# Optimization experiments

Measured on AMD Instinct MI355X. Metric: run time of the kernel, lower is better.

The kernel has to match this reference:

```python
import jax, jax.numpy as jnp
import numpy as np

TEMPERATURE = 0.5
NEG_FILL = -9000000000000000.0


def setup_inputs() -> dict:
    key = jax.random.key(0)
    k1, k2 = jax.random.split(key)
    z1 = jax.random.normal(k1, (4096, 256), dtype=jnp.float32)
    z2 = jax.random.normal(k2, (4096, 256), dtype=jnp.float32)
    return {"z1": z1, "z2": z2}


def reference(z1, z2):
    N = z1.shape[0]
    z = jnp.concatenate([z1, z2], axis=0)  # [2N, d]
    # cosine similarity: normalize once (eps matches torch's 1e-8) then GEMM
    norm = jnp.maximum(jnp.linalg.norm(z, axis=-1, keepdims=True), 1e-8)
    zn = z / norm
    sim = (zn @ zn.T) / TEMPERATURE  # [2N, 2N]
    # mask out self-similarity on the diagonal
    diag = jnp.eye(2 * N, dtype=bool)
    sim = jnp.where(diag, NEG_FILL, sim)
    labels = jnp.concatenate([jnp.arange(N) + N, jnp.arange(N)])  # positive pairs
    logp = jax.nn.log_softmax(sim, axis=-1)
    loss = -jnp.mean(jnp.take_along_axis(logp, labels[:, None], axis=1))
    return loss
```

## Files before the change

kernel.cpp:

```cpp
#include <hip/hip_runtime.h>
#include <hip/hip_bf16.h>


#define TWO_N 8192
#define NPAIR 4096
#define DDIM  256
#define NT    64
#define NBLK  (NT * (NT + 1) / 2)
#define INV_T 2.0f

typedef __attribute__((ext_vector_type(8))) short bf16x8;
typedef __attribute__((ext_vector_type(4))) float f32x4;

typedef __attribute__((address_space(1))) void gvoid_t;
typedef __attribute__((address_space(3))) void lvoid_t;

__device__ __forceinline__ void gload_lds16(const void* g, void* l) {
    __builtin_amdgcn_global_load_lds((gvoid_t*)g, (lvoid_t*)l, 16, 0, 0);
}

__global__ void k_normalize(const float* __restrict__ z1,
                            const float* __restrict__ z2,
                            __hip_bfloat16* __restrict__ zn,
                            float* __restrict__ e_diag,
                            float* __restrict__ pos,
                            float* __restrict__ row_sumexp,
                            float* __restrict__ out) {
    if (threadIdx.x < 8) row_sumexp[blockIdx.x * 8 + threadIdx.x] = 0.0f;
    if (blockIdx.x == 0 && threadIdx.x == 0) out[0] = 0.0f;

    const int w    = threadIdx.x >> 6;
    const int lane = threadIdx.x & 63;
    const int i    = blockIdx.x * 4 + w;

    float4 a = ((const float4*)(z1 + (size_t)i * DDIM))[lane];
    float4 b = ((const float4*)(z2 + (size_t)i * DDIM))[lane];

    float s1 = a.x * a.x + a.y * a.y + a.z * a.z + a.w * a.w;
    float s2 = b.x * b.x + b.y * b.y + b.z * b.z + b.w * b.w;
    float dd = a.x * b.x + a.y * b.y + a.z * b.z + a.w * b.w;
#pragma unroll
    for (int m = 1; m < 64; m <<= 1) {
        s1 += __shfl_xor(s1, m, 64);
        s2 += __shfl_xor(s2, m, 64);
        dd += __shfl_xor(dd, m, 64);
    }

    float inv1 = 1.0f / fmaxf(sqrtf(s1), 1e-8f);
    float inv2 = 1.0f / fmaxf(sqrtf(s2), 1e-8f);

    __hip_bfloat16 q1[4], q2[4];
    q1[0] = __float2bfloat16(a.x * inv1); q1[1] = __float2bfloat16(a.y * inv1);
    q1[2] = __float2bfloat16(a.z * inv1); q1[3] = __float2bfloat16(a.w * inv1);
    q2[0] = __float2bfloat16(b.x * inv2); q2[1] = __float2bfloat16(b.y * inv2);
    q2[2] = __float2bfloat16(b.z * inv2); q2[3] = __float2bfloat16(b.w * inv2);

    float qs1 = 0.0f, qs2 = 0.0f;
#pragma unroll
    for (int j = 0; j < 4; ++j) {
        float f1 = __bfloat162float(q1[j]);
        float f2 = __bfloat162float(q2[j]);
        qs1 += f1 * f1;
        qs2 += f2 * f2;
    }
#pragma unroll
    for (int m = 1; m < 64; m <<= 1) {
        qs1 += __shfl_xor(qs1, m, 64);
        qs2 += __shfl_xor(qs2, m, 64);
    }

    *reinterpret_cast<uint2*>(zn + (size_t)i * DDIM + lane * 4) =
        *reinterpret_cast<uint2*>(q1);
    *reinterpret_cast<uint2*>(zn + (size_t)(i + NPAIR) * DDIM + lane * 4) =
        *reinterpret_cast<uint2*>(q2);

    if (lane == 0) {
        e_diag[i]         = __expf(qs1 * INV_T);
        e_diag[i + NPAIR] = __expf(qs2 * INV_T);
        pos[i]            = dd * inv1 * inv2 * INV_T;
    }
}

__global__ __launch_bounds__(256, 2)
void k_gemm_sumexp(const __hip_bfloat16* __restrict__ zn,
                   float* __restrict__ row_sumexp) {
    __shared__ __align__(128) __hip_bfloat16 Asmem[128 * DDIM];

    const int tid  = threadIdx.x;
    const int lane = tid & 63;
    const int w    = tid >> 6;
    const int wr   = w >> 1;
    const int wc   = w & 1;
    const int lr   = lane & 15;
    const int quad = lane >> 4;

    int b = (blockIdx.x & 7) * (NBLK / 8) + (blockIdx.x >> 3);

    int rt = (int)(64.5f - sqrtf(64.5f * 64.5f - 2.0f * (float)b));
    if (rt < 0) rt = 0;
    if (rt > NT - 1) rt = NT - 1;
    while (rt > 0 && NT * rt - (rt * (rt - 1)) / 2 > b) --rt;
    while (NT * (rt + 1) - ((rt + 1) * rt) / 2 <= b) ++rt;
    const int ct   = rt + (b - (NT * rt - (rt * (rt - 1)) / 2));
    const bool diag = (rt == ct);

    const int row_base = rt * 128;
    const int col_base = ct * 128;

    const __hip_bfloat16* gB[4];
#pragma unroll
    for (int ni = 0; ni < 4; ++ni)
        gB[ni] = zn + (size_t)(col_base + wc * 64 + ni * 16 + lr) * DDIM + quad * 8;

    bf16x8 Bfr[8][4];
#pragma unroll
    for (int ks = 0; ks < 8; ++ks)
#pragma unroll
        for (int ni = 0; ni < 4; ++ni)
            Bfr[ks][ni] = *(const bf16x8*)(gB[ni] + ks * 32);

    {
        const int ck = (tid & 24) | ((tid & 7) ^ (tid >> 5));
        const char* gA = (const char*)(zn + (size_t)row_base * DDIM)
                       + (tid >> 5) * (DDIM * 2) + ck * 16;
        char* lA = (char*)Asmem + tid * 16;
#pragma unroll
        for (int j = 0; j < 16; ++j)
            gload_lds16(gA + (size_t)j * 8 * (DDIM * 2), lA + j * 4096);
    }
    __syncthreads();

    int pa[4];
#pragma unroll
    for (int mi = 0; mi < 4; ++mi)
        pa[mi] = (wr * 64 + mi * 16 + lr) * (DDIM * 2) + ((quad ^ (lr & 7)) << 4);

    f32x4 acc[4][4];
#pragma unroll
    for (int mi = 0; mi < 4; ++mi)
#pragma unroll
        for (int ni = 0; ni < 4; ++ni) acc[mi][ni] = (f32x4){0.f, 0.f, 0.f, 0.f};

    bf16x8 afc[4];
#pragma unroll
    for (int mi = 0; mi < 4; ++mi)
        afc[mi] = *(const bf16x8*)((const char*)Asmem + pa[mi]);

#pragma unroll
    for (int kstep = 0; kstep < 8; ++kstep) {
        bf16x8 afn[4];
        if (kstep < 7) {
            const int kn   = kstep + 1;
            const int koff = ((kn >> 1) << 7);
            const int kx   = ((kn & 1) << 6);
#pragma unroll
            for (int mi = 0; mi < 4; ++mi)
                afn[mi] = *(const bf16x8*)((const char*)Asmem + ((pa[mi] ^ kx) + koff));
        }
#pragma unroll
        for (int mi = 0; mi < 4; ++mi)
#pragma unroll
            for (int ni = 0; ni < 4; ++ni)
                acc[mi][ni] = __builtin_amdgcn_mfma_f32_16x16x32_bf16(
                    afc[mi], Bfr[kstep][ni], acc[mi][ni], 0, 0, 0);
        if (kstep < 7) {
#pragma unroll
            for (int mi = 0; mi < 4; ++mi) afc[mi] = afn[mi];
        }
    }

    float rs[4][4];
    float cs[4];
#pragma unroll
    for (int mi = 0; mi < 4; ++mi)
#pragma unroll
        for (int r = 0; r < 4; ++r) rs[mi][r] = 0.0f;
#pragma unroll
    for (int ni = 0; ni < 4; ++ni) cs[ni] = 0.0f;

#pragma unroll
    for (int mi = 0; mi < 4; ++mi)
#pragma unroll
        for (int ni = 0; ni < 4; ++ni)
#pragma unroll
            for (int r = 0; r < 4; ++r) {
                float e = __expf(acc[mi][ni][r] * INV_T);
                rs[mi][r] += e;
                cs[ni] += e;
            }

#pragma unroll
    for (int mi = 0; mi < 4; ++mi) {
#pragma unroll
        for (int r = 0; r < 4; ++r) {
            float v = rs[mi][r];
            v += __shfl_xor(v, 1, 64);
            v += __shfl_xor(v, 2, 64);
            v += __shfl_xor(v, 4, 64);
            v += __shfl_xor(v, 8, 64);
            if (lr == 0) {
                int row = row_base + wr * 64 + mi * 16 + quad * 4 + r;
                atomicAdd(&row_sumexp[row], v);
            }
        }
    }

    if (!diag) {
#pragma unroll
        for (int ni = 0; ni < 4; ++ni) {
            float v = cs[ni];
            v += __shfl_xor(v, 16, 64);
            v += __shfl_xor(v, 32, 64);
            if (quad == 0) {
                int col = col_base + wc * 64 + ni * 16 + lr;
                atomicAdd(&row_sumexp[col], v);
            }
        }
    }
}

__global__ void k_final(const float* __restrict__ row_sumexp,
                        const float* __restrict__ e_diag,
                        const float* __restrict__ pos,
                        float* __restrict__ out) {
    const int i    = blockIdx.x * 256 + threadIdx.x;
    const int w    = threadIdx.x >> 6;
    const int lane = threadIdx.x & 63;

    float t = logf(row_sumexp[i] - e_diag[i])
            + logf(row_sumexp[i + NPAIR] - e_diag[i + NPAIR])
            - 2.0f * pos[i];
#pragma unroll
    for (int m = 1; m < 64; m <<= 1) t += __shfl_xor(t, m, 64);

    __shared__ float ps[4];
    if (lane == 0) ps[w] = t;
    __syncthreads();
    if (threadIdx.x == 0) {
        float s = (ps[0] + ps[1] + ps[2] + ps[3]) * (1.0f / (float)TWO_N);
        atomicAdd(out, s);
    }
}

extern "C" void kernel_launch(void* const* d_in, const int* in_sizes, int n_in,
                              void* d_out, int out_size, void* d_ws, size_t ws_size,
                              hipStream_t stream) {
    const float* z1 = (const float*)d_in[0];
    const float* z2 = (const float*)d_in[1];
    float* out = (float*)d_out;

    char* ws = (char*)d_ws;
    __hip_bfloat16* zn  = (__hip_bfloat16*)ws;
    float* row_sumexp   = (float*)(ws + (size_t)TWO_N * DDIM * 2);
    float* e_diag       = row_sumexp + TWO_N;
    float* pos          = e_diag + TWO_N;

    k_normalize<<<NPAIR / 4, 256, 0, stream>>>(z1, z2, zn, e_diag, pos,
                                               row_sumexp, out);
    k_gemm_sumexp<<<NBLK, 256, 0, stream>>>(zn, row_sumexp);
    k_final<<<NPAIR / 256, 256, 0, stream>>>(row_sumexp, e_diag, pos, out);
}
```

Before: 126.0 us.

## Make GEMM-sumexp kernel persistent with A-tile reuse and overlapped epilogue

Replaces one-block-per-tile launch with a fixed grid of 256 persistent 512-thread blocks, each walking a contiguous range of upper-triangular tiles. The A row tile is restaged into LDS only when the row index changes, so consecutive tiles in the same row reuse it. The previous tile's exp/atomic epilogue runs while the next tile's B fragments load through inline asm global loads with manual waitcnt. This aims to cut launch and tail overhead and redundant A loads, at the cost of hand-tuned waitcnt assumptions and possible load imbalance across blocks.

```diff
diff --git a/kernel.cpp b/kernel.cpp
--- a/kernel.cpp
+++ b/kernel.cpp
@@ -8,6 +8,7 @@
 #define NT    64
 #define NBLK  (NT * (NT + 1) / 2)
 #define INV_T 2.0f
+#define GEMM_GRID 256
 
 typedef __attribute__((ext_vector_type(8))) short bf16x8;
 typedef __attribute__((ext_vector_type(4))) float f32x4;
@@ -81,7 +82,7 @@
     }
 }
 
-__global__ __launch_bounds__(256, 2)
+__global__ __launch_bounds__(512, 2)
 void k_gemm_sumexp(const __hip_bfloat16* __restrict__ zn,
                    float* __restrict__ row_sumexp) {
     __shared__ __align__(128) __hip_bfloat16 Asmem[128 * DDIM];
@@ -89,134 +90,155 @@
     const int tid  = threadIdx.x;
     const int lane = tid & 63;
     const int w    = tid >> 6;
-    const int wr   = w >> 1;
-    const int wc   = w & 1;
+    const int wr   = w >> 2;
+    const int wc   = w & 3;
     const int lr   = lane & 15;
     const int quad = lane >> 4;
 
-    int b = (blockIdx.x & 7) * (NBLK / 8) + (blockIdx.x >> 3);
-
+    const int t0 = (blockIdx.x * NBLK) >> 8;
+    const int t1 = ((blockIdx.x + 1) * NBLK) >> 8;
+
+    int b = t0;
     int rt = (int)(64.5f - sqrtf(64.5f * 64.5f - 2.0f * (float)b));
     if (rt < 0) rt = 0;
     if (rt > NT - 1) rt = NT - 1;
     while (rt > 0 && NT * rt - (rt * (rt - 1)) / 2 > b) --rt;
     while (NT * (rt + 1) - ((rt + 1) * rt) / 2 <= b) ++rt;
-    const int ct   = rt + (b - (NT * rt - (rt * (rt - 1)) / 2));
-    const bool diag = (rt == ct);
-
-    const int row_base = rt * 128;
-    const int col_base = ct * 128;
-
-    const __hip_bfloat16* gB[4];
-#pragma unroll
-    for (int ni = 0; ni < 4; ++ni)
-        gB[ni] = zn + (size_t)(col_base + wc * 64 + ni * 16 + lr) * DDIM + quad * 8;
-
-    bf16x8 Bfr[8][4];
-#pragma unroll
-    for (int ks = 0; ks < 8; ++ks)
-#pragma unroll
-        for (int ni = 0; ni < 4; ++ni)
-            Bfr[ks][ni] = *(const bf16x8*)(gB[ni] + ks * 32);
-
-    {
-        const int ck = (tid & 24) | ((tid & 7) ^ (tid >> 5));
-        const char* gA = (const char*)(zn + (size_t)row_base * DDIM)
-                       + (tid >> 5) * (DDIM * 2) + ck * 16;
-        char* lA = (char*)Asmem + tid * 16;
-#pragma unroll
-        for (int j = 0; j < 16; ++j)
-            gload_lds16(gA + (size_t)j * 8 * (DDIM * 2), lA + j * 4096);
-    }
-    __syncthreads();
-
-    int pa[4];
-#pragma unroll
-    for (int mi = 0; mi < 4; ++mi)
-        pa[mi] = (wr * 64 + mi * 16 + lr) * (DDIM * 2) + ((quad ^ (lr & 7)) << 4);
-
-    f32x4 acc[4][4];
-#pragma unroll
-    for (int mi = 0; mi < 4; ++mi)
-#pragma unroll
-        for (int ni = 0; ni < 4; ++ni) acc[mi][ni] = (f32x4){0.f, 0.f, 0.f, 0.f};
-
-    bf16x8 afc[4];
-#pragma unroll
-    for (int mi = 0; mi < 4; ++mi)
-        afc[mi] = *(const bf16x8*)((const char*)Asmem + pa[mi]);
-
-#pragma unroll
-    for (int kstep = 0; kstep < 8; ++kstep) {
-        bf16x8 afn[4];
-        if (kstep < 7) {
-            const int kn   = kstep + 1;
-            const int koff = ((kn >> 1) << 7);
-            const int kx   = ((kn & 1) << 6);
+    int ct = rt + (b - (NT * rt - (rt * (rt - 1)) / 2));
+
+    int cur_rt = -1;
+    f32x4 acc[4][2];
+    int  pRow = 0, pCol = 0;
+    bool pDiag = false, havePrev = false;
+
+    auto epilogue = [&]() {
+        float rs[4][4], cs[2];
+#pragma unroll
+        for (int mi = 0; mi < 4; ++mi)
+#pragma unroll
+            for (int r = 0; r < 4; ++r) rs[mi][r] = 0.0f;
+        cs[0] = cs[1] = 0.0f;
+#pragma unroll
+        for (int mi = 0; mi < 4; ++mi)
+#pragma unroll
+            for (int ni = 0; ni < 2; ++ni)
+#pragma unroll
+                for (int r = 0; r < 4; ++r) {
+                    float e = __expf(acc[mi][ni][r] * INV_T);
+                    rs[mi][r] += e;
+                    cs[ni] += e;
+                }
+#pragma unroll
+        for (int mi = 0; mi < 4; ++mi)
+#pragma unroll
+            for (int r = 0; r < 4; ++r) {
+                float v = rs[mi][r];
+                v += __shfl_xor(v, 1, 64);
+                v += __shfl_xor(v, 2, 64);
+                v += __shfl_xor(v, 4, 64);
+                v += __shfl_xor(v, 8, 64);
+                if (lr == 0)
+                    atomicAdd(&row_sumexp[pRow + wr * 64 + mi * 16 + quad * 4 + r], v);
+            }
+        if (!pDiag) {
+#pragma unroll
+            for (int ni = 0; ni < 2; ++ni) {
+                float v = cs[ni];
+                v += __shfl_xor(v, 16, 64);
+                v += __shfl_xor(v, 32, 64);
+                if (quad == 0)
+                    atomicAdd(&row_sumexp[pCol + wc * 32 + ni * 16 + lr], v);
+            }
+        }
+    };
+
+    for (int t = t0; t < t1; ++t) {
+        const int  row_base = rt * 128;
+        const int  col_base = ct * 128;
+        const bool diag     = (rt == ct);
+        const bool restage  = (rt != cur_rt);
+
+        if (restage) {
+            __syncthreads();
+            const int ck = (tid & 24) | ((tid & 7) ^ ((tid >> 5) & 7));
+            const char* gA = (const char*)(zn + (size_t)row_base * DDIM)
+                           + (tid >> 5) * (DDIM * 2) + ck * 16;
+            char* lA = (char*)Asmem + tid * 16;
+#pragma unroll
+            for (int j = 0; j < 8; ++j)
+                gload_lds16(gA + (size_t)j * 16 * (DDIM * 2), lA + j * 8192);
+            cur_rt = rt;
+        }
+
+        const __hip_bfloat16* gB0 =
+            zn + (size_t)(col_base + wc * 32 + lr) * DDIM + quad * 8;
+        bf16x8 Bfr[8][2];
+#pragma unroll
+        for (int ks = 0; ks < 8; ++ks) {
+            const __hip_bfloat16* p0 = gB0 + ks * 32;
+            const __hip_bfloat16* p1 = p0 + 16 * DDIM;
+            asm volatile("global_load_dwordx4 %0, %1, off"
+                         : "=v"(Bfr[ks][0]) : "v"(p0) : "memory");
+            asm volatile("global_load_dwordx4 %0, %1, off"
+                         : "=v"(Bfr[ks][1]) : "v"(p1) : "memory");
+        }
+
+        if (havePrev) epilogue();
+        havePrev = true; pRow = row_base; pCol = col_base; pDiag = diag;
+
+        int pa[4];
+#pragma unroll
+        for (int mi = 0; mi < 4; ++mi)
+            pa[mi] = (wr * 64 + mi * 16 + lr) * (DDIM * 2) + ((quad ^ (lr & 7)) << 4);
+
+        bf16x8 afc[4];
+        if (restage) {
+            asm volatile("s_waitcnt vmcnt(0)" ::: "memory");
+            __syncthreads();
 #pragma unroll
             for (int mi = 0; mi < 4; ++mi)
-                afn[mi] = *(const bf16x8*)((const char*)Asmem + ((pa[mi] ^ kx) + koff));
-        }
-#pragma unroll
-        for (int mi = 0; mi < 4; ++mi)
-#pragma unroll
-            for (int ni = 0; ni < 4; ++ni)
-                acc[mi][ni] = __builtin_amdgcn_mfma_f32_16x16x32_bf16(
-                    afc[mi], Bfr[kstep][ni], acc[mi][ni], 0, 0, 0);
-        if (kstep < 7) {
-#pragma unroll
-            for (int mi = 0; mi < 4; ++mi) afc[mi] = afn[mi];
-        }
-    }
-
-    float rs[4][4];
-    float cs[4];
-#pragma unroll
-    for (int mi = 0; mi < 4; ++mi)
-#pragma unroll
-        for (int r = 0; r < 4; ++r) rs[mi][r] = 0.0f;
-#pragma unroll
-    for (int ni = 0; ni < 4; ++ni) cs[ni] = 0.0f;
-
-#pragma unroll
-    for (int mi = 0; mi < 4; ++mi)
-#pragma unroll
-        for (int ni = 0; ni < 4; ++ni)
-#pragma unroll
-            for (int r = 0; r < 4; ++r) {
-                float e = __expf(acc[mi][ni][r] * INV_T);
-                rs[mi][r] += e;
-                cs[ni] += e;
-            }
-
-#pragma unroll
-    for (int mi = 0; mi < 4; ++mi) {
-#pragma unroll
-        for (int r = 0; r < 4; ++r) {
-            float v = rs[mi][r];
-            v += __shfl_xor(v, 1, 64);
-            v += __shfl_xor(v, 2, 64);
-            v += __shfl_xor(v, 4, 64);
-            v += __shfl_xor(v, 8, 64);
-            if (lr == 0) {
-                int row = row_base + wr * 64 + mi * 16 + quad * 4 + r;
-                atomicAdd(&row_sumexp[row], v);
-            }
-        }
-    }
-
-    if (!diag) {
-#pragma unroll
-        for (int ni = 0; ni < 4; ++ni) {
-            float v = cs[ni];
-            v += __shfl_xor(v, 16, 64);
-            v += __shfl_xor(v, 32, 64);
-            if (quad == 0) {
-                int col = col_base + wc * 64 + ni * 16 + lr;
-                atomicAdd(&row_sumexp[col], v);
-            }
-        }
-    }
+                afc[mi] = *(const bf16x8*)((const char*)Asmem + pa[mi]);
+        } else {
+#pragma unroll
+            for (int mi = 0; mi < 4; ++mi)
+                afc[mi] = *(const bf16x8*)((const char*)Asmem + pa[mi]);
+            asm volatile("s_waitcnt vmcnt(16)" ::: "memory");
+        }
+        __builtin_amdgcn_sched_barrier(0);
+
+#pragma unroll
+        for (int mi = 0; mi < 4; ++mi)
+#pragma unroll
+            for (int ni = 0; ni < 2; ++ni)
+                acc[mi][ni] = (f32x4){0.f, 0.f, 0.f, 0.f};
+
+#pragma unroll
+        for (int kstep = 0; kstep < 8; ++kstep) {
+            bf16x8 afn[4];
+            if (kstep < 7) {
+                const int kn   = kstep + 1;
+                const int koff = (kn >> 1) << 7;
+                const int kx   = (kn & 1) << 6;
+#pragma unroll
+                for (int mi = 0; mi < 4; ++mi)
+                    afn[mi] = *(const bf16x8*)((const char*)Asmem + ((pa[mi] ^ kx) + koff));
+            }
+#pragma unroll
+            for (int mi = 0; mi < 4; ++mi)
+#pragma unroll
+                for (int ni = 0; ni < 2; ++ni)
+                    acc[mi][ni] = __builtin_amdgcn_mfma_f32_16x16x32_bf16(
+                        afc[mi], Bfr[kstep][ni], acc[mi][ni], 0, 0, 0);
+            if (kstep < 7) {
+#pragma unroll
+                for (int mi = 0; mi < 4; ++mi) afc[mi] = afn[mi];
+            }
+        }
+
+        if (++ct >= NT) { ++rt; ct = rt; }
+    }
+
+    epilogue();
 }
 
 __global__ void k_final(const float* __restrict__ row_sumexp,
@@ -257,6 +279,6 @@
 
     k_normalize<<<NPAIR / 4, 256, 0, stream>>>(z1, z2, zn, e_diag, pos,
                                                row_sumexp, out);
-    k_gemm_sumexp<<<NBLK, 256, 0, stream>>>(zn, row_sumexp);
+    k_gemm_sumexp<<<GEMM_GRID, 512, 0, stream>>>(zn, row_sumexp);
     k_final<<<NPAIR / 256, 256, 0, stream>>>(row_sumexp, e_diag, pos, out);
 }
```

Result: slower. 128.6 us (+2.1%).
